# Kernel optimization log

Hardware: AMD Instinct MI355X
Metric: run time of the kernel (lower is better)

## Reference

```python
import jax, jax.numpy as jnp
import numpy as np

D_MODEL = 1024
N_HEADS = 16
D_K = D_MODEL // N_HEADS
B, L = 4, 2048


def setup_inputs() -> dict:
    key = jax.random.key(0)
    ks = jax.random.split(key, 9)
    s = 1.0 / np.sqrt(D_MODEL)
    return {
        "x": jax.random.normal(ks[0], (B, L, D_MODEL), dtype=jnp.float32),
        "mask": jnp.ones((B, L), dtype=jnp.int32),
        "Wq": jax.random.uniform(ks[1], (D_MODEL, D_MODEL), jnp.float32, -s, s),
        "bq": jax.random.uniform(ks[2], (D_MODEL,), jnp.float32, -s, s),
        "Wk": jax.random.uniform(ks[3], (D_MODEL, D_MODEL), jnp.float32, -s, s),
        "bk": jax.random.uniform(ks[4], (D_MODEL,), jnp.float32, -s, s),
        "Wv": jax.random.uniform(ks[5], (D_MODEL, D_MODEL), jnp.float32, -s, s),
        "bv": jax.random.uniform(ks[6], (D_MODEL,), jnp.float32, -s, s),
        "Wo": jax.random.uniform(ks[7], (D_MODEL, D_MODEL), jnp.float32, -s, s),
        "bo": jax.random.uniform(ks[8], (D_MODEL,), jnp.float32, -s, s),
    }


def reference(x, mask, Wq, bq, Wk, bk, Wv, bv, Wo, bo):
    b, l, d = x.shape
    # project and split heads: [B, H, L, d_k]
    def heads(W, bias):
        return (x @ W.T + bias).reshape(b, l, N_HEADS, D_K).transpose(0, 2, 1, 3)
    Q = heads(Wq, bq)
    K = heads(Wk, bk)
    V = heads(Wv, bv)
    scores = jnp.einsum("bhqd,bhkd->bhqk", Q, K) / np.sqrt(D_K).astype(np.float32)
    # mask: [B, L] -> broadcast over heads and query dim as [B, 1, 1, L]
    scores = jnp.where(mask[:, None, None, :] == 0, jnp.float32(-1e9), scores)
    attn = jax.nn.softmax(scores, axis=-1)  # dropout=0 in eval math
    out = jnp.einsum("bhqk,bhkd->bhqd", attn, V)
    out = out.transpose(0, 2, 1, 3).reshape(b, l, d)
    return out @ Wo.T + bo
```

## Files before the change

### kernel.cpp

```cpp
#include <hip/hip_runtime.h>
#include <stdint.h>

#define DMODEL 1024
#define NHEADS 16
#define DK     64
#define BATCH  4
#define SEQ    2048
#define MROWS  (BATCH*SEQ)

typedef __bf16 bf16x8 __attribute__((ext_vector_type(8)));
typedef float  f32x4  __attribute__((ext_vector_type(4)));

#if defined(__has_builtin)
#if __has_builtin(__builtin_amdgcn_exp2f)
#define EXP2F(x) __builtin_amdgcn_exp2f(x)
#endif
#endif
#ifndef EXP2F
#define EXP2F(x) exp2f(x)
#endif

__device__ __forceinline__ unsigned short f2bf(float f) {
    unsigned int u = __builtin_bit_cast(unsigned int, f);
    u += 0x7fffu + ((u >> 16) & 1u);
    return (unsigned short)(u >> 16);
}

__device__ __forceinline__ unsigned int pack_bf16(float a, float b) {
    unsigned int ua = __builtin_bit_cast(unsigned int, a) + 0x8000u;
    unsigned int ub = __builtin_bit_cast(unsigned int, b) + 0x8000u;
    return __builtin_amdgcn_perm(ub, ua, 0x07060302u);
}

#define GLDS(gp, lp) __builtin_amdgcn_global_load_lds( \
    (const __attribute__((address_space(1))) unsigned int*)(gp), \
    (__attribute__((address_space(3))) unsigned int*)(lp), 16, 0, 0)

__global__ void cvt_kernel(const float* __restrict__ src,
                           unsigned short* __restrict__ dst, int n4) {
    int i = blockIdx.x * blockDim.x + threadIdx.x;
    if (i >= n4) return;
    const float4 v = reinterpret_cast<const float4*>(src)[i];
    ushort4 o;
    o.x = f2bf(v.x); o.y = f2bf(v.y); o.z = f2bf(v.z); o.w = f2bf(v.w);
    reinterpret_cast<ushort4*>(dst)[i] = o;
}

__global__ void cvtw_kernel(const float* __restrict__ w0, const float* __restrict__ w1,
                            const float* __restrict__ w2, const float* __restrict__ w3,
                            unsigned short* __restrict__ d0, unsigned short* __restrict__ d1,
                            unsigned short* __restrict__ d2, unsigned short* __restrict__ d3) {
    const float* s; unsigned short* d;
    switch (blockIdx.y) {
        case 0:  s = w0; d = d0; break;
        case 1:  s = w1; d = d1; break;
        case 2:  s = w2; d = d2; break;
        default: s = w3; d = d3; break;
    }
    const int i = blockIdx.x * blockDim.x + threadIdx.x;
    const float4 v = reinterpret_cast<const float4*>(s)[i];
    ushort4 o;
    o.x = f2bf(v.x); o.y = f2bf(v.y); o.z = f2bf(v.z); o.w = f2bf(v.w);
    reinterpret_cast<ushort4*>(d)[i] = o;
}

__global__ void maskbias_kernel(const int* __restrict__ m, float* __restrict__ o, int n) {
    const int i = blockIdx.x * blockDim.x + threadIdx.x;
    if (i < n) o[i] = m[i] ? 0.f : -1e30f;
}

template<int MODE>
__global__ __launch_bounds__(256, 3) void gemm128(
        const unsigned short* __restrict__ A,
        const unsigned short* __restrict__ W0,
        const unsigned short* __restrict__ W1,
        const unsigned short* __restrict__ W2,
        const float* __restrict__ b0,
        const float* __restrict__ b1,
        const float* __restrict__ b2,
        void* __restrict__ o0, void* __restrict__ o1, void* __restrict__ o2) {
    __shared__ unsigned short As[128 * 64];
    __shared__ unsigned short Bs[128 * 64];
    const int lane = threadIdx.x & 63;
    const int wave = threadIdx.x >> 6;
    const int quad = lane >> 4;
    const int r15  = lane & 15;
    const int wr = wave >> 1, wc = wave & 1;
    const int m0 = blockIdx.y * 128;

    int which, ncol0;
    const unsigned short* W;
    const float* bias;
    if (MODE == 0) {
        which = blockIdx.x >> 3;
        ncol0 = (blockIdx.x & 7) * 128;
        W    = which == 0 ? W0 : (which == 1 ? W1 : W2);
        bias = which == 0 ? b0 : (which == 1 ? b1 : b2);
    } else {
        which = 0; ncol0 = blockIdx.x * 128; W = W0; bias = b0;
    }

    const int srow = lane >> 3;
    const int scg  = (lane & 7) ^ srow;
    const unsigned short* Ag[4];
    const unsigned short* Wg[4];
    #pragma unroll
    for (int j = 0; j < 4; ++j) {
        const int row = (wave * 4 + j) * 8 + srow;
        Ag[j] = A + (m0 + row) * DMODEL + scg * 8;
        Wg[j] = W + (ncol0 + row) * DMODEL + scg * 8;
    }

    f32x4 acc[4][4] = {};
    for (int kk = 0; kk < DMODEL; kk += 64) {
        __syncthreads();
        #pragma unroll
        for (int j = 0; j < 4; ++j) {
            GLDS(Ag[j] + kk, &As[(wave * 4 + j) * 512]);
            GLDS(Wg[j] + kk, &Bs[(wave * 4 + j) * 512]);
        }
        __syncthreads();
        #pragma unroll
        for (int u = 0; u < 2; ++u) {
            bf16x8 af[4], bfx[4];
            const int cs = ((u * 4 + quad) ^ (r15 & 7)) * 8;
            #pragma unroll
            for (int t = 0; t < 4; ++t) {
                af[t]  = *(const bf16x8*)&As[(wr * 64 + t * 16 + r15) * 64 + cs];
                bfx[t] = *(const bf16x8*)&Bs[(wc * 64 + t * 16 + r15) * 64 + cs];
            }
            #pragma unroll
            for (int mt = 0; mt < 4; ++mt)
                #pragma unroll
                for (int nt = 0; nt < 4; ++nt)
                    acc[mt][nt] = __builtin_amdgcn_mfma_f32_16x16x32_bf16(
                        af[mt], bfx[nt], acc[mt][nt], 0, 0, 0);
        }
    }

    #pragma unroll
    for (int mt = 0; mt < 4; ++mt) {
        #pragma unroll
        for (int nt = 0; nt < 4; ++nt) {
            #pragma unroll
            for (int r = 0; r < 4; ++r) {
                const int row = m0 + wr * 64 + mt * 16 + quad * 4 + r;
                const int col = ncol0 + wc * 64 + nt * 16 + r15;
                float v = acc[mt][nt][r] + bias[col];
                if (MODE == 1) {
                    ((float*)o0)[(size_t)row * DMODEL + col] = v;
                } else {
                    if (which == 0) v *= 0.18033688011112042f;
                    const int b = row >> 11, l = row & (SEQ - 1);
                    const int h = col >> 6,  d = col & (DK - 1);
                    const int bh = b * NHEADS + h;
                    unsigned short* ow = (unsigned short*)(which == 0 ? o0 : (which == 1 ? o1 : o2));
                    size_t idx;
                    if (which < 2) idx = ((size_t)bh * SEQ + l) * DK + d;
                    else           idx = (size_t)bh * (SEQ * DK) + (l >> 6) * (DK * 64) + d * 64 + (l & 63);
                    ow[idx] = f2bf(v);
                }
            }
        }
    }
}

__global__ __launch_bounds__(256, 4) void flash_attn(
        const unsigned short* __restrict__ Q,
        const unsigned short* __restrict__ Km,
        const unsigned short* __restrict__ Vm,
        const float* __restrict__ mbf,
        unsigned short* __restrict__ Oa) {
    __shared__ unsigned short Ks[64 * 64];
    __shared__ unsigned short Vs[64 * 64];
    __shared__ unsigned short Pl[4][2][16 * 64];
    const int lane = threadIdx.x & 63;
    const int wave = threadIdx.x >> 6;
    const int quad = lane >> 4;
    const int r15  = lane & 15;

    const int id   = (blockIdx.y << 4) | blockIdx.x;
    const int xcd  = id & 7;
    const int slot = id >> 3;
    const int bh   = xcd + ((slot >> 4) << 3);
    const int qt   = slot & 15;
    const int b = bh >> 4, h = bh & (NHEADS - 1);
    const int q0 = qt * 128 + wave * 32;

    const unsigned short* Qb = Q  + (size_t)bh * SEQ * DK;
    const unsigned short* Kb = Km + (size_t)bh * SEQ * DK;
    const unsigned short* Vb = Vm + (size_t)bh * SEQ * DK;
    const float* mb = mbf + b * SEQ;

    const int srow = lane >> 3;
    const int soff = ((lane >> 3) * 64) + (((lane & 7) ^ srow) * 8);

    bf16x8 bq[2][2];
    #pragma unroll
    for (int qf = 0; qf < 2; ++qf)
        #pragma unroll
        for (int u = 0; u < 2; ++u)
            bq[qf][u] = *(const bf16x8*)(Qb + (q0 + qf * 16 + r15) * DK + u * 32 + quad * 8);

    float l_part[2] = {0.f, 0.f};
    f32x4 oacc[2][4] = {};

    for (int kb = 0; kb < SEQ; kb += 64) {
        __syncthreads();
        const unsigned short* Kg = Kb + kb * 64;
        const unsigned short* Vg = Vb + kb * 64;
        #pragma unroll
        for (int j = 0; j < 2; ++j) {
            const int wseg = wave * 2 + j;
            GLDS(Kg + wseg * 512 + soff, &Ks[wseg * 512]);
            GLDS(Vg + wseg * 512 + soff, &Vs[wseg * 512]);
        }
        __syncthreads();

        char* const Pb = (char*)&Pl[wave][0][0];
        #pragma unroll
        for (int t = 0; t < 4; ++t) {
            const bf16x8 ak0 = *(const bf16x8*)&Ks[(t * 16 + r15) * 64 + ((quad ^ (r15 & 7)) * 8)];
            const bf16x8 ak1 = *(const bf16x8*)&Ks[(t * 16 + r15) * 64 + (((4 + quad) ^ (r15 & 7)) * 8)];
            const float4 m4 = *(const float4*)(mb + kb + t * 16 + quad * 4);
            #pragma unroll
            for (int qf = 0; qf < 2; ++qf) {
                f32x4 z = {};
                z = __builtin_amdgcn_mfma_f32_16x16x32_bf16(ak0, bq[qf][0], z, 0, 0, 0);
                z = __builtin_amdgcn_mfma_f32_16x16x32_bf16(ak1, bq[qf][1], z, 0, 0, 0);
                const float p0 = EXP2F(z[0] + m4.x);
                const float p1 = EXP2F(z[1] + m4.y);
                const float p2 = EXP2F(z[2] + m4.z);
                const float p3 = EXP2F(z[3] + m4.w);
                l_part[qf] += (p0 + p1) + (p2 + p3);
                uint2 pw;
                pw.x = pack_bf16(p0, p1);
                pw.y = pack_bf16(p2, p3);
                const int c2 = (t * 2 + (quad >> 1)) ^ (r15 & 7);
                *(uint2*)(Pb + qf * 2048 + r15 * 128 + c2 * 16 + (quad & 1) * 8) = pw;
            }
        }
        asm volatile("s_waitcnt lgkmcnt(0)" ::: "memory");

        #pragma unroll
        for (int u = 0; u < 2; ++u) {
            const int cs = ((u * 4 + quad) ^ (r15 & 7)) * 8;
            bf16x8 vf[4];
            #pragma unroll
            for (int nt = 0; nt < 4; ++nt)
                vf[nt] = *(const bf16x8*)&Vs[(nt * 16 + r15) * 64 + cs];
            #pragma unroll
            for (int qf = 0; qf < 2; ++qf) {
                const bf16x8 ap = *(const bf16x8*)(Pb + qf * 2048 + r15 * 128 + cs * 2);
                #pragma unroll
                for (int nt = 0; nt < 4; ++nt)
                    oacc[qf][nt] = __builtin_amdgcn_mfma_f32_16x16x32_bf16(
                        ap, vf[nt], oacc[qf][nt], 0, 0, 0);
            }
        }
    }

    #pragma unroll
    for (int qf = 0; qf < 2; ++qf) {
        float l = l_part[qf];
        l += __shfl_xor(l, 16);
        l += __shfl_xor(l, 32);
        float lq[4];
        #pragma unroll
        for (int r = 0; r < 4; ++r) lq[r] = __shfl(l, quad * 4 + r, 64);
        #pragma unroll
        for (int nt = 0; nt < 4; ++nt) {
            #pragma unroll
            for (int r = 0; r < 4; ++r) {
                const int row = q0 + qf * 16 + quad * 4 + r;
                const int col = h * DK + nt * 16 + r15;
                Oa[((size_t)b * SEQ + row) * DMODEL + col] = f2bf(oacc[qf][nt][r] / lq[r]);
            }
        }
    }
}

extern "C" void kernel_launch(void* const* d_in, const int* in_sizes, int n_in,
                              void* d_out, int out_size, void* d_ws, size_t ws_size,
                              hipStream_t stream) {
    (void)in_sizes; (void)n_in; (void)out_size; (void)ws_size;
    const float* x  = (const float*)d_in[0];
    const int* mask = (const int*)d_in[1];
    const float* Wq = (const float*)d_in[2];
    const float* bq = (const float*)d_in[3];
    const float* Wk = (const float*)d_in[4];
    const float* bk = (const float*)d_in[5];
    const float* Wv = (const float*)d_in[6];
    const float* bv = (const float*)d_in[7];
    const float* Wo = (const float*)d_in[8];
    const float* bo = (const float*)d_in[9];
    float* out = (float*)d_out;

    char* ws = (char*)d_ws;
    unsigned short* xb  = (unsigned short*)(ws);
    unsigned short* wqb = (unsigned short*)(ws + 16777216);
    unsigned short* wkb = (unsigned short*)(ws + 16777216 + 1 * 2097152);
    unsigned short* wvb = (unsigned short*)(ws + 16777216 + 2 * 2097152);
    unsigned short* wob = (unsigned short*)(ws + 16777216 + 3 * 2097152);
    unsigned short* qb  = (unsigned short*)(ws + 16777216 + 4 * 2097152);
    unsigned short* kb  = qb  + (size_t)MROWS * DMODEL;
    unsigned short* vtb = kb  + (size_t)MROWS * DMODEL;
    unsigned short* ab  = vtb + (size_t)MROWS * DMODEL;
    float*          mbf = (float*)(ab + (size_t)MROWS * DMODEL);

    cvt_kernel<<<dim3(MROWS * DMODEL / 4 / 256), 256, 0, stream>>>(x, xb, MROWS * DMODEL / 4);
    cvtw_kernel<<<dim3(DMODEL * DMODEL / 4 / 256, 4), 256, 0, stream>>>(
        Wq, Wk, Wv, Wo, wqb, wkb, wvb, wob);
    maskbias_kernel<<<dim3(BATCH * SEQ / 256), 256, 0, stream>>>(mask, mbf, BATCH * SEQ);

    gemm128<0><<<dim3(24, MROWS / 128), 256, 0, stream>>>(
        xb, wqb, wkb, wvb, bq, bk, bv, qb, kb, vtb);

    flash_attn<<<dim3(16, BATCH * NHEADS), 256, 0, stream>>>(qb, kb, vtb, mbf, ab);

    gemm128<1><<<dim3(8, MROWS / 128), 256, 0, stream>>>(
        ab, wob, nullptr, nullptr, bo, nullptr, nullptr, out, nullptr, nullptr);
}
```

Measured before the change: 301.3 us.

## Keep P in registers via f16 MFMA and vectorize GEMM/attention epilogues

Flash attention no longer spills the P tile to LDS. P is packed to fp16 in registers and fed to 16x16x16 f16 MFMAs with V stored as fp16, which removes an LDS round trip and the wait between the two stages. The projection GEMMs swap MFMA operands so each lane holds contiguous columns, allowing vectorized bias loads and 8/16-byte stores. Conversion kernels use packed bf16 stores, and the softmax normalization uses a reciprocal multiply. This trades V and P precision from bf16 to fp16, uses round-toward-zero packing, and relies on an approximate reciprocal.

Result: slower. 414.3 us (+37.5%).

```diff
diff --git a/kernel.cpp b/kernel.cpp
--- a/kernel.cpp
+++ b/kernel.cpp
@@ -8,8 +8,10 @@
 #define SEQ    2048
 #define MROWS  (BATCH*SEQ)
 
-typedef __bf16 bf16x8 __attribute__((ext_vector_type(8)));
-typedef float  f32x4  __attribute__((ext_vector_type(4)));
+typedef __bf16   bf16x8 __attribute__((ext_vector_type(8)));
+typedef float    f32x4  __attribute__((ext_vector_type(4)));
+typedef _Float16 f16x4  __attribute__((ext_vector_type(4)));
+typedef _Float16 f16x2  __attribute__((ext_vector_type(2)));
 
 #if defined(__has_builtin)
 #if __has_builtin(__builtin_amdgcn_exp2f)
@@ -31,6 +33,9 @@
     unsigned int ub = __builtin_bit_cast(unsigned int, b) + 0x8000u;
     return __builtin_amdgcn_perm(ub, ua, 0x07060302u);
 }
+__device__ __forceinline__ unsigned int pack_f16(float a, float b) {
+    return __builtin_bit_cast(unsigned int, __builtin_amdgcn_cvt_pkrtz(a, b));
+}
 
 #define GLDS(gp, lp) __builtin_amdgcn_global_load_lds( \
     (const __attribute__((address_space(1))) unsigned int*)(gp), \
@@ -41,9 +46,10 @@
     int i = blockIdx.x * blockDim.x + threadIdx.x;
     if (i >= n4) return;
     const float4 v = reinterpret_cast<const float4*>(src)[i];
-    ushort4 o;
-    o.x = f2bf(v.x); o.y = f2bf(v.y); o.z = f2bf(v.z); o.w = f2bf(v.w);
-    reinterpret_cast<ushort4*>(dst)[i] = o;
+    uint2 o;
+    o.x = pack_bf16(v.x, v.y);
+    o.y = pack_bf16(v.z, v.w);
+    reinterpret_cast<uint2*>(dst)[i] = o;
 }
 
 __global__ void cvtw_kernel(const float* __restrict__ w0, const float* __restrict__ w1,
@@ -59,9 +65,10 @@
     }
     const int i = blockIdx.x * blockDim.x + threadIdx.x;
     const float4 v = reinterpret_cast<const float4*>(s)[i];
-    ushort4 o;
-    o.x = f2bf(v.x); o.y = f2bf(v.y); o.z = f2bf(v.z); o.w = f2bf(v.w);
-    reinterpret_cast<ushort4*>(d)[i] = o;
+    uint2 o;
+    o.x = pack_bf16(v.x, v.y);
+    o.y = pack_bf16(v.z, v.w);
+    reinterpret_cast<uint2*>(d)[i] = o;
 }
 
 __global__ void maskbias_kernel(const int* __restrict__ m, float* __restrict__ o, int n) {
@@ -111,7 +118,12 @@
         Wg[j] = W + (ncol0 + row) * DMODEL + scg * 8;
     }
 
+    const bool ct = (MODE == 1) || (MODE == 0 &&  false) || false;
+    const bool swap_ops = (MODE == 1) || (MODE == 0 ? true : false);
+    (void)ct; (void)swap_ops;
+
     f32x4 acc[4][4] = {};
+    const bool use_ct = (MODE == 1) || (which < 2);
     for (int kk = 0; kk < DMODEL; kk += 64) {
         __syncthreads();
         #pragma unroll
@@ -129,12 +141,21 @@
                 af[t]  = *(const bf16x8*)&As[(wr * 64 + t * 16 + r15) * 64 + cs];
                 bfx[t] = *(const bf16x8*)&Bs[(wc * 64 + t * 16 + r15) * 64 + cs];
             }
-            #pragma unroll
-            for (int mt = 0; mt < 4; ++mt)
+            if (use_ct) {
                 #pragma unroll
-                for (int nt = 0; nt < 4; ++nt)
-                    acc[mt][nt] = __builtin_amdgcn_mfma_f32_16x16x32_bf16(
-                        af[mt], bfx[nt], acc[mt][nt], 0, 0, 0);
+                for (int mt = 0; mt < 4; ++mt)
+                    #pragma unroll
+                    for (int nt = 0; nt < 4; ++nt)
+                        acc[mt][nt] = __builtin_amdgcn_mfma_f32_16x16x32_bf16(
+                            bfx[nt], af[mt], acc[mt][nt], 0, 0, 0);
+            } else {
+                #pragma unroll
+                for (int mt = 0; mt < 4; ++mt)
+                    #pragma unroll
+                    for (int nt = 0; nt < 4; ++nt)
+                        acc[mt][nt] = __builtin_amdgcn_mfma_f32_16x16x32_bf16(
+                            af[mt], bfx[nt], acc[mt][nt], 0, 0, 0);
+            }
         }
     }
 
@@ -142,24 +163,52 @@
     for (int mt = 0; mt < 4; ++mt) {
         #pragma unroll
         for (int nt = 0; nt < 4; ++nt) {
-            #pragma unroll
-            for (int r = 0; r < 4; ++r) {
-                const int row = m0 + wr * 64 + mt * 16 + quad * 4 + r;
-                const int col = ncol0 + wc * 64 + nt * 16 + r15;
-                float v = acc[mt][nt][r] + bias[col];
-                if (MODE == 1) {
-                    ((float*)o0)[(size_t)row * DMODEL + col] = v;
-                } else {
-                    if (which == 0) v *= 0.18033688011112042f;
-                    const int b = row >> 11, l = row & (SEQ - 1);
-                    const int h = col >> 6,  d = col & (DK - 1);
-                    const int bh = b * NHEADS + h;
-                    unsigned short* ow = (unsigned short*)(which == 0 ? o0 : (which == 1 ? o1 : o2));
-                    size_t idx;
-                    if (which < 2) idx = ((size_t)bh * SEQ + l) * DK + d;
-                    else           idx = (size_t)bh * (SEQ * DK) + (l >> 6) * (DK * 64) + d * 64 + (l & 63);
-                    ow[idx] = f2bf(v);
+            if (MODE == 1) {
+                const int row  = m0 + wr * 64 + mt * 16 + r15;
+                const int col0 = ncol0 + wc * 64 + nt * 16 + quad * 4;
+                const float4 b4 = *(const float4*)&bias[col0];
+                float4 v;
+                v.x = acc[mt][nt][0] + b4.x;
+                v.y = acc[mt][nt][1] + b4.y;
+                v.z = acc[mt][nt][2] + b4.z;
+                v.w = acc[mt][nt][3] + b4.w;
+                *(float4*)&((float*)o0)[(size_t)row * DMODEL + col0] = v;
+            } else if (which < 2) {
+                const int row  = m0 + wr * 64 + mt * 16 + r15;
+                const int col0 = ncol0 + wc * 64 + nt * 16 + quad * 4;
+                const float4 b4 = *(const float4*)&bias[col0];
+                float v0 = acc[mt][nt][0] + b4.x;
+                float v1 = acc[mt][nt][1] + b4.y;
+                float v2 = acc[mt][nt][2] + b4.z;
+                float v3 = acc[mt][nt][3] + b4.w;
+                if (which == 0) {
+                    const float sc = 0.18033688011112042f;
+                    v0 *= sc; v1 *= sc; v2 *= sc; v3 *= sc;
                 }
+                const int b = row >> 11, l = row & (SEQ - 1);
+                const int h = col0 >> 6, d0 = col0 & (DK - 1);
+                const int bh = b * NHEADS + h;
+                unsigned short* ow = (unsigned short*)(which == 0 ? o0 : o1);
+                uint2 pw;
+                pw.x = pack_bf16(v0, v1);
+                pw.y = pack_bf16(v2, v3);
+                *(uint2*)&ow[((size_t)bh * SEQ + l) * DK + d0] = pw;
+            } else {
+                const int row0 = m0 + wr * 64 + mt * 16 + quad * 4;
+                const int col  = ncol0 + wc * 64 + nt * 16 + r15;
+                const float bb = bias[col];
+                const float v0 = acc[mt][nt][0] + bb;
+                const float v1 = acc[mt][nt][1] + bb;
+                const float v2 = acc[mt][nt][2] + bb;
+                const float v3 = acc[mt][nt][3] + bb;
+                const int b = row0 >> 11, l0 = row0 & (SEQ - 1);
+                const int h = col >> 6, d = col & (DK - 1);
+                const int bh = b * NHEADS + h;
+                uint2 pw;
+                pw.x = pack_f16(v0, v1);
+                pw.y = pack_f16(v2, v3);
+                unsigned short* ow = (unsigned short*)o2;
+                *(uint2*)&ow[(size_t)bh * (SEQ * DK) + (l0 >> 6) * (DK * 64) + d * 64 + (l0 & 63)] = pw;
             }
         }
     }
@@ -173,7 +222,6 @@
         unsigned short* __restrict__ Oa) {
     __shared__ unsigned short Ks[64 * 64];
     __shared__ unsigned short Vs[64 * 64];
-    __shared__ unsigned short Pl[4][2][16 * 64];
     const int lane = threadIdx.x & 63;
     const int wave = threadIdx.x >> 6;
     const int quad = lane >> 4;
@@ -193,7 +241,7 @@
     const float* mb = mbf + b * SEQ;
 
     const int srow = lane >> 3;
-    const int soff = ((lane >> 3) * 64) + (((lane & 7) ^ srow) * 8);
+    const int soff = (srow * 64) + (((lane & 7) ^ srow) * 8);
 
     bf16x8 bq[2][2];
     #pragma unroll
@@ -217,7 +265,7 @@
         }
         __syncthreads();
 
-        char* const Pb = (char*)&Pl[wave][0][0];
+        f16x4 pfrag[4][2];
         #pragma unroll
         for (int t = 0; t < 4; ++t) {
             const bf16x8 ak0 = *(const bf16x8*)&Ks[(t * 16 + r15) * 64 + ((quad ^ (r15 & 7)) * 8)];
@@ -234,28 +282,22 @@
                 const float p3 = EXP2F(z[3] + m4.w);
                 l_part[qf] += (p0 + p1) + (p2 + p3);
                 uint2 pw;
-                pw.x = pack_bf16(p0, p1);
-                pw.y = pack_bf16(p2, p3);
-                const int c2 = (t * 2 + (quad >> 1)) ^ (r15 & 7);
-                *(uint2*)(Pb + qf * 2048 + r15 * 128 + c2 * 16 + (quad & 1) * 8) = pw;
-            }
-        }
-        asm volatile("s_waitcnt lgkmcnt(0)" ::: "memory");
-
-        #pragma unroll
-        for (int u = 0; u < 2; ++u) {
-            const int cs = ((u * 4 + quad) ^ (r15 & 7)) * 8;
-            bf16x8 vf[4];
+                pw.x = pack_f16(p0, p1);
+                pw.y = pack_f16(p2, p3);
+                pfrag[t][qf] = __builtin_bit_cast(f16x4, pw);
+            }
+        }
+
+        #pragma unroll
+        for (int nt = 0; nt < 4; ++nt) {
             #pragma unroll
-            for (int nt = 0; nt < 4; ++nt)
-                vf[nt] = *(const bf16x8*)&Vs[(nt * 16 + r15) * 64 + cs];
-            #pragma unroll
-            for (int qf = 0; qf < 2; ++qf) {
-                const bf16x8 ap = *(const bf16x8*)(Pb + qf * 2048 + r15 * 128 + cs * 2);
+            for (int t = 0; t < 4; ++t) {
+                const int chunk = (2 * t + (quad >> 1)) ^ (r15 & 7);
+                const f16x4 vf = *(const f16x4*)&Vs[(nt * 16 + r15) * 64 + chunk * 8 + (quad & 1) * 4];
                 #pragma unroll
-                for (int nt = 0; nt < 4; ++nt)
-                    oacc[qf][nt] = __builtin_amdgcn_mfma_f32_16x16x32_bf16(
-                        ap, vf[nt], oacc[qf][nt], 0, 0, 0);
+                for (int qf = 0; qf < 2; ++qf)
+                    oacc[qf][nt] = __builtin_amdgcn_mfma_f32_16x16x16f16(
+                        vf, pfrag[t][qf], oacc[qf][nt], 0, 0, 0);
             }
         }
     }
@@ -265,17 +307,15 @@
         float l = l_part[qf];
         l += __shfl_xor(l, 16);
         l += __shfl_xor(l, 32);
-        float lq[4];
-        #pragma unroll
-        for (int r = 0; r < 4; ++r) lq[r] = __shfl(l, quad * 4 + r, 64);
+        const float rl = __builtin_amdgcn_rcpf(l);
+        const int row = q0 + qf * 16 + r15;
         #pragma unroll
         for (int nt = 0; nt < 4; ++nt) {
-            #pragma unroll
-            for (int r = 0; r < 4; ++r) {
-                const int row = q0 + qf * 16 + quad * 4 + r;
-                const int col = h * DK + nt * 16 + r15;
-                Oa[((size_t)b * SEQ + row) * DMODEL + col] = f2bf(oacc[qf][nt][r] / lq[r]);
-            }
+            const int col0 = h * DK + nt * 16 + quad * 4;
+            uint2 pw;
+            pw.x = pack_bf16(oacc[qf][nt][0] * rl, oacc[qf][nt][1] * rl);
+            pw.y = pack_bf16(oacc[qf][nt][2] * rl, oacc[qf][nt][3] * rl);
+            *(uint2*)&Oa[((size_t)b * SEQ + row) * DMODEL + col0] = pw;
         }
     }
 }
```
